# Kernel optimization log

Measured on AMD Instinct MI355X. Metric: run time of the kernel, lower is better.

The kernel has to match this reference:

```python
import jax, jax.numpy as jnp
import numpy as np
from jax import lax

BN_EPS = 1e-5

def conv_bn_silu(x, w, g, b, m, v):
    # 3x3 conv, stride 1, pad 1, no bias (NCHW / OIHW)
    y = lax.conv_general_dilated(x, w, window_strides=(1, 1),
                                 padding=((1, 1), (1, 1)),
                                 dimension_numbers=('NCHW', 'OIHW', 'NCHW'))
    scale = (g / jnp.sqrt(v + BN_EPS))[None, :, None, None]
    shift = (b - m * g / jnp.sqrt(v + BN_EPS))[None, :, None, None]
    y = y * scale + shift
    return y * jax.nn.sigmoid(y)  # SiLU


def setup_inputs() -> dict:
    key = jax.random.key(0)
    ks = jax.random.split(key, 11)
    B, C, H, W = 2, 512, 64, 64
    Ck = 64
    x = jax.random.normal(ks[0], (B, C, H, W), dtype=jnp.float32)
    w1 = jax.random.normal(ks[1], (Ck, C, 3, 3), dtype=jnp.float32) * 0.02
    g1 = jax.random.uniform(ks[2], (Ck,), dtype=jnp.float32) + 0.5
    b1 = jax.random.normal(ks[3], (Ck,), dtype=jnp.float32) * 0.1
    m1 = jax.random.normal(ks[4], (Ck,), dtype=jnp.float32) * 0.1
    v1 = jax.random.uniform(ks[5], (Ck,), dtype=jnp.float32) * 0.5 + 0.5
    w2 = jax.random.normal(ks[6], (Ck, C, 3, 3), dtype=jnp.float32) * 0.02
    g2 = jax.random.uniform(ks[7], (Ck,), dtype=jnp.float32) + 0.5
    b2 = jax.random.normal(ks[8], (Ck,), dtype=jnp.float32) * 0.1
    m2 = jax.random.normal(ks[9], (Ck,), dtype=jnp.float32) * 0.1
    v2 = jax.random.uniform(ks[10], (Ck,), dtype=jnp.float32) * 0.5 + 0.5
    return {"x": x, "w1": w1, "g1": g1, "b1": b1, "m1": m1, "v1": v1,
            "w2": w2, "g2": g2, "b2": b2, "m2": m2, "v2": v2}


def reference(x, w1, g1, b1, m1, v1, w2, g2, b2, m2, v2):
    B, C, H, W = x.shape
    y1 = conv_bn_silu(x, w1, g1, b1, m1, v1)  # [B,64,H,W]
    y2 = conv_bn_silu(x, w2, g2, b2, m2, v2)  # [B,64,H,W]
    x_ = x.reshape(B, C, H * W)               # [B,512,N]
    y1_ = y1.reshape(B, y1.shape[1], H * W)   # [B,64,N]
    y2_ = y2.reshape(B, y2.shape[1], H * W)   # [B,64,N]
    # c[b,n,m] = sum_k y2[b,k,n] * y1[b,k,m]  (no scaling)
    c = jnp.einsum('bkn,bkm->bnm', y2_, y1_)
    cw = jax.nn.softmax(c, axis=-1)           # [B,N,N]
    out = jnp.einsum('bcn,bnm->bcm', x_, cw)  # [B,512,N]
    return out.reshape(B, C, H, W)
```

## Files before the change

### kernel.cpp

```cpp
#include <hip/hip_runtime.h>

#define BN_EPS 1e-5f
#define B_ 2
#define C_ 512
#define CK_ 64
#define N_ 4096

typedef unsigned short u16;
typedef _Float16 half8 __attribute__((ext_vector_type(8)));
typedef _Float16 half4 __attribute__((ext_vector_type(4)));
typedef float f32x4 __attribute__((ext_vector_type(4)));

static __device__ inline u16 h2u(_Float16 h) {
    union { _Float16 h; u16 u; } x; x.h = h; return x.u;
}

__global__ __launch_bounds__(256) void prep_weights_kernel(
    const float* __restrict__ w1, const float* __restrict__ g1, const float* __restrict__ b1,
    const float* __restrict__ m1, const float* __restrict__ v1,
    const float* __restrict__ w2, const float* __restrict__ g2, const float* __restrict__ b2,
    const float* __restrict__ m2, const float* __restrict__ v2,
    u16* __restrict__ wh, float* __restrict__ shiftA)
{
    int idx = blockIdx.x * 256 + threadIdx.x;
    int c   = idx & 511;
    int co  = (idx >> 9) & 63;
    int tap = (idx >> 15) % 9;
    int j   = idx / (9 << 15);
    const float* w = j ? w2 : w1;
    const float* g = j ? g2 : g1;
    const float* v = j ? v2 : v1;
    float scale = g[co] / sqrtf(v[co] + BN_EPS);
    float val = w[((size_t)co * C_ + c) * 9 + tap] * scale;
    wh[idx] = h2u((_Float16)val);
    if (idx < 2 * CK_) {
        int jj = idx >> 6, cc = idx & 63;
        const float* gg = jj ? g2 : g1;
        const float* vv = jj ? v2 : v1;
        const float* bb = jj ? b2 : b1;
        const float* mm = jj ? m2 : m1;
        float sc = gg[cc] / sqrtf(vv[cc] + BN_EPS);
        shiftA[idx] = bb[cc] - mm[cc] * sc;
    }
}

__global__ __launch_bounds__(256) void cast_x_kernel(
    const float* __restrict__ x, u16* __restrict__ xh)
{
    int i = (blockIdx.x * 256 + threadIdx.x) * 8;
    float4 v0 = *(const float4*)(x + i);
    float4 v1 = *(const float4*)(x + i + 4);
    half8 h;
    h[0] = (_Float16)v0.x; h[1] = (_Float16)v0.y; h[2] = (_Float16)v0.z; h[3] = (_Float16)v0.w;
    h[4] = (_Float16)v1.x; h[5] = (_Float16)v1.y; h[6] = (_Float16)v1.z; h[7] = (_Float16)v1.w;
    *(half8*)(void*)(xh + i) = h;
}

__global__ __launch_bounds__(256) void transpose_x_kernel(
    const float* __restrict__ x, u16* __restrict__ xt)
{
    int blk = blockIdx.x;
    int nb = blk & 15;
    int kg = (blk >> 4) & 7;
    int b  = blk >> 7;
    int n = nb * 256 + threadIdx.x;
    const float* sp = x + (size_t)b * C_ * N_ + n;
    u16* dp = xt + ((size_t)(b * N_ + n)) * C_;
    #pragma unroll
    for (int kc = 0; kc < 8; ++kc) {
        int c0 = kg * 64 + kc * 8;
        half8 h;
        #pragma unroll
        for (int q = 0; q < 8; ++q)
            h[q] = (_Float16)sp[(size_t)(c0 + q) * N_];
        *(half8*)(void*)(dp + c0) = h;
    }
}

__global__ __launch_bounds__(512) void conv_mfma_kernel(
    const u16* __restrict__ xt, const u16* __restrict__ wh,
    const float* __restrict__ shiftA,
    u16* __restrict__ y1t, u16* __restrict__ y2t)
{
    __shared__ __align__(16) _Float16 xs[3 * 66 * 40];
    __shared__ __align__(16) _Float16 wsm[9 * 64 * 40];
    int blk = blockIdx.x;
    int h = blk & 63;
    int j = (blk >> 6) & 1;
    int b = blk >> 7;
    int t = threadIdx.x;
    int wave = t >> 6, lane = t & 63;
    int l16 = lane & 15, kk = lane >> 4;
    int w0  = (wave & 3) * 16;
    int co0 = (wave >> 2) * 32;

    const u16* xtb = xt + (size_t)b * N_ * C_;
    const u16* whj = wh + (size_t)j * 9 * 64 * C_;

    f32x4 acc[2] = {};

    for (int cc = 0; cc < 16; ++cc) {
        __syncthreads();
        for (int i = t; i < 792; i += 512) {
            int c8 = i & 3;
            int wi = (i >> 2) % 66;
            int r  = i / 264;
            int row = h - 1 + r;
            half8 v = {};
            if (row >= 0 && row < 64 && wi >= 1 && wi <= 64)
                v = *(const half8*)(const void*)(xtb
                      + ((size_t)(row * 64 + wi - 1)) * C_ + cc * 32 + c8 * 8);
            *(half8*)(void*)&xs[(r * 66 + wi) * 40 + c8 * 8] = v;
        }
        for (int i = t; i < 2304; i += 512) {
            int c8 = i & 3;
            int co = (i >> 2) & 63;
            int tap = i >> 8;
            *(half8*)(void*)&wsm[(tap * 64 + co) * 40 + c8 * 8] =
                *(const half8*)(const void*)(whj
                    + ((size_t)(tap * 64 + co)) * C_ + cc * 32 + c8 * 8);
        }
        __syncthreads();
        #pragma unroll
        for (int tap = 0; tap < 9; ++tap) {
            int dh = tap / 3, dw = tap - dh * 3;
            int wi = w0 + l16 + dw;
            half8 a  = *(const half8*)(const void*)&xs[(dh * 66 + wi) * 40 + kk * 8];
            half8 b0 = *(const half8*)(const void*)&wsm[(tap * 64 + co0 + l16) * 40 + kk * 8];
            half8 b1 = *(const half8*)(const void*)&wsm[(tap * 64 + co0 + 16 + l16) * 40 + kk * 8];
            acc[0] = __builtin_amdgcn_mfma_f32_16x16x32_f16(a, b0, acc[0], 0, 0, 0);
            acc[1] = __builtin_amdgcn_mfma_f32_16x16x32_f16(a, b1, acc[1], 0, 0, 0);
        }
    }
    u16* yt = (j ? y2t : y1t) + (size_t)b * N_ * 64;
    #pragma unroll
    for (int nt = 0; nt < 2; ++nt) {
        float sh = shiftA[j * 64 + co0 + nt * 16 + l16];
        #pragma unroll
        for (int r = 0; r < 4; ++r) {
            float yv = acc[nt][r] + sh;
            float sg = 1.f / (1.f + __expf(-yv));
            int n = h * 64 + w0 + kk * 4 + r;
            yt[(size_t)n * 64 + co0 + nt * 16 + l16] = h2u((_Float16)(yv * sg));
        }
    }
}

__global__ __launch_bounds__(256) void stats_mfma_kernel(
    const u16* __restrict__ y1t, const u16* __restrict__ y2t,
    float* __restrict__ part)
{
    int blk = blockIdx.x;
    int mc = blk & 3;
    int nt = (blk >> 2) & 63;
    int b  = blk >> 8;
    int n0 = nt * 64;
    int t = threadIdx.x;
    int w = t >> 6, lane = t & 63;
    int l16 = lane & 15, kk = lane >> 4;
    const u16* yt1b = y1t + (size_t)b * N_ * CK_;
    const u16* yt2b = y2t + (size_t)b * N_ * CK_;

    int nw = n0 + w * 16;
    const u16* ap = yt2b + (size_t)(nw + l16) * CK_ + kk * 8;
    half8 a0 = *(const half8*)(const void*)ap;
    half8 a1 = *(const half8*)(const void*)(ap + 32);

    float rmax[4] = {-3.0e38f, -3.0e38f, -3.0e38f, -3.0e38f};
    float rsum[4] = {0.f, 0.f, 0.f, 0.f};
    int mbase = mc * 1024;

    for (int mi = 0; mi < 16; ++mi) {
        int m0 = mbase + mi * 64;
        #pragma unroll
        for (int ms = 0; ms < 4; ++ms) {
            const u16* bp = yt1b + (size_t)(m0 + ms * 16 + l16) * CK_ + kk * 8;
            half8 b0 = *(const half8*)(const void*)bp;
            half8 b1 = *(const half8*)(const void*)(bp + 32);
            f32x4 acc = {0.f, 0.f, 0.f, 0.f};
            acc = __builtin_amdgcn_mfma_f32_16x16x32_f16(a0, b0, acc, 0, 0, 0);
            acc = __builtin_amdgcn_mfma_f32_16x16x32_f16(a1, b1, acc, 0, 0, 0);
            #pragma unroll
            for (int r = 0; r < 4; ++r) {
                float c = acc[r];
                float M = fmaxf(rmax[r], c);
                rsum[r] = rsum[r] * __expf(rmax[r] - M) + __expf(c - M);
                rmax[r] = M;
            }
        }
    }
    #pragma unroll
    for (int r = 0; r < 4; ++r) {
        float M = rmax[r], S = rsum[r];
        #pragma unroll
        for (int d = 1; d < 16; d <<= 1) {
            float Mo = __shfl_xor(M, d, 64);
            float So = __shfl_xor(S, d, 64);
            float Mn = fmaxf(M, Mo);
            S = S * __expf(M - Mn) + So * __expf(Mo - Mn);
            M = Mn;
        }
        if (l16 == 0) {
            int n = nw + kk * 4 + r;
            size_t o = (((size_t)b * 4 + mc) * N_ + n) * 2;
            part[o]     = M;
            part[o + 1] = S;
        }
    }
}

__global__ __launch_bounds__(256) void stats_final_kernel(
    const float* __restrict__ part, float* __restrict__ rowmax, float* __restrict__ rowinv)
{
    int i = blockIdx.x * 256 + threadIdx.x;
    if (i >= B_ * N_) return;
    int b = i / N_, n = i % N_;
    float M = -3.0e38f, S = 0.f;
    #pragma unroll
    for (int c = 0; c < 4; ++c) {
        size_t o = (((size_t)b * 4 + c) * N_ + n) * 2;
        float Mc = part[o], Sc = part[o + 1];
        float Mn = fmaxf(M, Mc);
        S = S * __expf(M - Mn) + Sc * __expf(Mc - Mn);
        M = Mn;
    }
    rowmax[i] = M;
    rowinv[i] = 1.f / S;
}

__global__ __launch_bounds__(256, 4) void attn_fused_kernel(
    const u16* __restrict__ xh, const u16* __restrict__ y1t, const u16* __restrict__ y2t,
    const float* __restrict__ rowmax, const float* __restrict__ rowinv,
    float* __restrict__ out)
{
    __shared__ __align__(16) _Float16 xls[128 * 64];
    __shared__ __align__(16) _Float16 pls[64 * 72];
    int gid = blockIdx.x;
    int blk = (gid & 7) * 64 + (gid >> 3);
    int mb = blk & 63;
    int cb = (blk >> 6) & 3;
    int b  = blk >> 8;
    int c0 = cb * 128, m0 = mb * 64;
    int t = threadIdx.x;
    int w = t >> 6, lane = t & 63;
    int l16 = lane & 15, kk = lane >> 4;

    const u16* xb   = xh  + (size_t)b * C_ * N_;
    const u16* y1b  = y1t + (size_t)b * N_ * 64;
    const u16* y2b  = y2t + (size_t)b * N_ * 64;
    const float* Mrow = rowmax + b * N_;
    const float* Irow = rowinv + b * N_;

    half8 By[4][2];
    #pragma unroll
    for (int ms = 0; ms < 4; ++ms)
        #pragma unroll
        for (int g = 0; g < 2; ++g)
            By[ms][g] = *(const half8*)(const void*)(y1b
                + (size_t)(m0 + ms * 16 + l16) * 64 + g * 32 + kk * 8);

    f32x4 acc[2][4] = {};

    for (int nc = 0; nc < 64; ++nc) {
        __syncthreads();
        #pragma unroll
        for (int rd = 0; rd < 4; ++rd) {
            int sbase = rd * 256 + w * 64;
            int s = sbase + lane;
            int r = s >> 3, c8 = s & 7;
            const u16* gsrc = xb + (size_t)(c0 + r) * N_ + nc * 64 + ((c8 ^ (r & 7)) * 8);
            __builtin_amdgcn_global_load_lds(
                (const __attribute__((address_space(1))) void*)gsrc,
                (__attribute__((address_space(3))) void*)((char*)xls + sbase * 16),
                16, 0, 0);
        }
        {
            const u16* ap = y2b + (size_t)(nc * 64 + w * 16 + l16) * 64 + kk * 8;
            half8 a0 = *(const half8*)(const void*)ap;
            half8 a1 = *(const half8*)(const void*)(ap + 32);
            float Mr[4], Ir[4];
            #pragma unroll
            for (int r = 0; r < 4; ++r) {
                int n = nc * 64 + w * 16 + kk * 4 + r;
                Mr[r] = Mrow[n]; Ir[r] = Irow[n];
            }
            #pragma unroll
            for (int ms = 0; ms < 4; ++ms) {
                f32x4 pa = {0.f, 0.f, 0.f, 0.f};
                pa = __builtin_amdgcn_mfma_f32_16x16x32_f16(a0, By[ms][0], pa, 0, 0, 0);
                pa = __builtin_amdgcn_mfma_f32_16x16x32_f16(a1, By[ms][1], pa, 0, 0, 0);
                int mloc = ms * 16 + l16;
                half4 pv;
                #pragma unroll
                for (int r = 0; r < 4; ++r)
                    pv[r] = (_Float16)(__expf(pa[r] - Mr[r]) * Ir[r]);
                *(half4*)(void*)&pls[mloc * 72 + w * 16 + kk * 4] = pv;
            }
        }
        __syncthreads();
        #pragma unroll
        for (int g = 0; g < 2; ++g) {
            half8 Ax[2];
            #pragma unroll
            for (int ci = 0; ci < 2; ++ci) {
                int row = w * 32 + ci * 16 + l16;
                int q8 = (g * 4 + kk) ^ (row & 7);
                Ax[ci] = *(const half8*)(const void*)&xls[row * 64 + q8 * 8];
            }
            half8 Bp[4];
            #pragma unroll
            for (int mi = 0; mi < 4; ++mi) {
                int mloc = mi * 16 + l16;
                Bp[mi] = *(const half8*)(const void*)&pls[mloc * 72 + g * 32 + kk * 8];
            }
            #pragma unroll
            for (int ci = 0; ci < 2; ++ci)
                #pragma unroll
                for (int mi = 0; mi < 4; ++mi)
                    acc[ci][mi] = __builtin_amdgcn_mfma_f32_16x16x32_f16(
                        Ax[ci], Bp[mi], acc[ci][mi], 0, 0, 0);
        }
    }
    #pragma unroll
    for (int ci = 0; ci < 2; ++ci)
        #pragma unroll
        for (int mi = 0; mi < 4; ++mi)
            #pragma unroll
            for (int r = 0; r < 4; ++r)
                out[(size_t)(b * C_ + c0 + w * 32 + ci * 16 + kk * 4 + r) * N_
                    + m0 + mi * 16 + l16] = acc[ci][mi][r];
}

extern "C" void kernel_launch(void* const* d_in, const int* in_sizes, int n_in,
                              void* d_out, int out_size, void* d_ws, size_t ws_size,
                              hipStream_t stream) {
    const float* x  = (const float*)d_in[0];
    const float* w1 = (const float*)d_in[1];
    const float* g1 = (const float*)d_in[2];
    const float* b1 = (const float*)d_in[3];
    const float* m1 = (const float*)d_in[4];
    const float* v1 = (const float*)d_in[5];
    const float* w2 = (const float*)d_in[6];
    const float* g2 = (const float*)d_in[7];
    const float* b2 = (const float*)d_in[8];
    const float* m2 = (const float*)d_in[9];
    const float* v2 = (const float*)d_in[10];
    float* out = (float*)d_out;

    constexpr size_t SHIFT_N = 2ULL * CK_;
    constexpr size_t ROW_N   = (size_t)B_ * N_;
    constexpr size_t PART_N  = (size_t)B_ * 4 * N_ * 2;
    constexpr size_t WH_N    = 2ULL * 9 * CK_ * C_;
    constexpr size_t XH_N    = (size_t)B_ * C_ * N_;
    constexpr size_t YT_N    = (size_t)B_ * N_ * CK_;

    float* ws = (float*)d_ws;
    float* shiftA = ws;
    float* rowmax = shiftA + SHIFT_N;
    float* rowinv = rowmax + ROW_N;
    float* part   = rowinv + ROW_N;
    float* f32_end = part + PART_N;
    u16*   wh     = (u16*)f32_end;
    u16*   xh     = wh + WH_N;
    u16*   xt     = xh + XH_N;
    u16*   y1t    = xt + XH_N;
    u16*   y2t    = y1t + YT_N;
    (void)ws_size; (void)in_sizes; (void)n_in; (void)out_size;

    prep_weights_kernel<<<2304, 256, 0, stream>>>(w1, g1, b1, m1, v1,
                                                  w2, g2, b2, m2, v2, wh, shiftA);
    cast_x_kernel<<<2048, 256, 0, stream>>>(x, xh);
    transpose_x_kernel<<<256, 256, 0, stream>>>(x, xt);
    conv_mfma_kernel<<<256, 512, 0, stream>>>(xt, wh, shiftA, y1t, y2t);
    stats_mfma_kernel<<<512, 256, 0, stream>>>(y1t, y2t, part);
    stats_final_kernel<<<32, 256, 0, stream>>>(part, rowmax, rowinv);
    attn_fused_kernel<<<512, 256, 0, stream>>>(xh, y1t, y2t, rowmax, rowinv, out);
}
```

Baseline: 274.9 us.

## Double-buffer x tile and P tile in fused attention loop

Doubles the LDS buffers for the x tile and the probability tile so that the async load and softmax-probability computation for the next chunk overlap with the MFMA accumulation of the current chunk. This cuts the two barriers per iteration down to one. The y2 fragment for the chunk after next is prefetched into registers. Launch bounds drop from 4 to 2 blocks per SM to make room for the doubled LDS (about 52KB per block) and the extra registers, which lowers occupancy.

```diff
diff --git a/kernel.cpp b/kernel.cpp
--- a/kernel.cpp
+++ b/kernel.cpp
@@ -228,13 +228,13 @@
     rowinv[i] = 1.f / S;
 }
 
-__global__ __launch_bounds__(256, 4) void attn_fused_kernel(
+__global__ __launch_bounds__(256, 2) void attn_fused_kernel(
     const u16* __restrict__ xh, const u16* __restrict__ y1t, const u16* __restrict__ y2t,
     const float* __restrict__ rowmax, const float* __restrict__ rowinv,
     float* __restrict__ out)
 {
-    __shared__ __align__(16) _Float16 xls[128 * 64];
-    __shared__ __align__(16) _Float16 pls[64 * 72];
+    __shared__ __align__(16) _Float16 xls[2][128 * 64];
+    __shared__ __align__(16) _Float16 pls[2][64 * 72];
     int gid = blockIdx.x;
     int blk = (gid & 7) * 64 + (gid >> 3);
     int mb = blk & 63;
@@ -259,10 +259,12 @@
             By[ms][g] = *(const half8*)(const void*)(y1b
                 + (size_t)(m0 + ms * 16 + l16) * 64 + g * 32 + kk * 8);
 
-    f32x4 acc[2][4] = {};
-
-    for (int nc = 0; nc < 64; ++nc) {
-        __syncthreads();
+    auto load_a = [&](int nc, half8& a0, half8& a1) {
+        const u16* ap = y2b + (size_t)(nc * 64 + w * 16 + l16) * 64 + kk * 8;
+        a0 = *(const half8*)(const void*)ap;
+        a1 = *(const half8*)(const void*)(ap + 32);
+    };
+    auto stage_x = [&](int buf, int nc) {
         #pragma unroll
         for (int rd = 0; rd < 4; ++rd) {
             int sbase = rd * 256 + w * 64;
@@ -271,33 +273,33 @@
             const u16* gsrc = xb + (size_t)(c0 + r) * N_ + nc * 64 + ((c8 ^ (r & 7)) * 8);
             __builtin_amdgcn_global_load_lds(
                 (const __attribute__((address_space(1))) void*)gsrc,
-                (__attribute__((address_space(3))) void*)((char*)xls + sbase * 16),
+                (__attribute__((address_space(3))) void*)((char*)&xls[buf][0] + sbase * 16),
                 16, 0, 0);
         }
-        {
-            const u16* ap = y2b + (size_t)(nc * 64 + w * 16 + l16) * 64 + kk * 8;
-            half8 a0 = *(const half8*)(const void*)ap;
-            half8 a1 = *(const half8*)(const void*)(ap + 32);
-            float Mr[4], Ir[4];
-            #pragma unroll
-            for (int r = 0; r < 4; ++r) {
-                int n = nc * 64 + w * 16 + kk * 4 + r;
-                Mr[r] = Mrow[n]; Ir[r] = Irow[n];
-            }
-            #pragma unroll
-            for (int ms = 0; ms < 4; ++ms) {
-                f32x4 pa = {0.f, 0.f, 0.f, 0.f};
-                pa = __builtin_amdgcn_mfma_f32_16x16x32_f16(a0, By[ms][0], pa, 0, 0, 0);
-                pa = __builtin_amdgcn_mfma_f32_16x16x32_f16(a1, By[ms][1], pa, 0, 0, 0);
-                int mloc = ms * 16 + l16;
-                half4 pv;
-                #pragma unroll
-                for (int r = 0; r < 4; ++r)
-                    pv[r] = (_Float16)(__expf(pa[r] - Mr[r]) * Ir[r]);
-                *(half4*)(void*)&pls[mloc * 72 + w * 16 + kk * 4] = pv;
-            }
-        }
-        __syncthreads();
+    };
+    auto compute_p = [&](int buf, int nc, half8 a0, half8 a1) {
+        float Mr[4], Ir[4];
+        #pragma unroll
+        for (int r = 0; r < 4; ++r) {
+            int n = nc * 64 + w * 16 + kk * 4 + r;
+            Mr[r] = Mrow[n]; Ir[r] = Irow[n];
+        }
+        #pragma unroll
+        for (int ms = 0; ms < 4; ++ms) {
+            f32x4 pa = {0.f, 0.f, 0.f, 0.f};
+            pa = __builtin_amdgcn_mfma_f32_16x16x32_f16(a0, By[ms][0], pa, 0, 0, 0);
+            pa = __builtin_amdgcn_mfma_f32_16x16x32_f16(a1, By[ms][1], pa, 0, 0, 0);
+            int mloc = ms * 16 + l16;
+            half4 pv;
+            #pragma unroll
+            for (int r = 0; r < 4; ++r)
+                pv[r] = (_Float16)(__expf(pa[r] - Mr[r]) * Ir[r]);
+            *(half4*)(void*)&pls[buf][mloc * 72 + w * 16 + kk * 4] = pv;
+        }
+    };
+
+    f32x4 acc[2][4] = {};
+    auto phase2 = [&](int buf) {
         #pragma unroll
         for (int g = 0; g < 2; ++g) {
             half8 Ax[2];
@@ -305,13 +307,13 @@
             for (int ci = 0; ci < 2; ++ci) {
                 int row = w * 32 + ci * 16 + l16;
                 int q8 = (g * 4 + kk) ^ (row & 7);
-                Ax[ci] = *(const half8*)(const void*)&xls[row * 64 + q8 * 8];
+                Ax[ci] = *(const half8*)(const void*)&xls[buf][row * 64 + q8 * 8];
             }
             half8 Bp[4];
             #pragma unroll
             for (int mi = 0; mi < 4; ++mi) {
                 int mloc = mi * 16 + l16;
-                Bp[mi] = *(const half8*)(const void*)&pls[mloc * 72 + g * 32 + kk * 8];
+                Bp[mi] = *(const half8*)(const void*)&pls[buf][mloc * 72 + g * 32 + kk * 8];
             }
             #pragma unroll
             for (int ci = 0; ci < 2; ++ci)
@@ -320,7 +322,28 @@
                     acc[ci][mi] = __builtin_amdgcn_mfma_f32_16x16x32_f16(
                         Ax[ci], Bp[mi], acc[ci][mi], 0, 0, 0);
         }
-    }
+    };
+
+    half8 a0c, a1c, a0n, a1n;
+    load_a(0, a0c, a1c);
+    stage_x(0, 0);
+    compute_p(0, 0, a0c, a1c);
+    load_a(1, a0n, a1n);
+    __syncthreads();
+
+    for (int nc = 0; nc < 63; ++nc) {
+        int cur = nc & 1;
+        stage_x(cur ^ 1, nc + 1);
+        compute_p(cur ^ 1, nc + 1, a0n, a1n);
+        int pf = (nc + 2 > 63) ? 63 : nc + 2;
+        half8 t0, t1;
+        load_a(pf, t0, t1);
+        phase2(cur);
+        __syncthreads();
+        a0n = t0; a1n = t1;
+    }
+    phase2(1);
+
     #pragma unroll
     for (int ci = 0; ci < 2; ++ci)
         #pragma unroll
```

Result: faster. 249.2 us (-9.4%).
